# Performance work log

Measured on AMD Instinct MI355X. Metric: run time of the kernel, lower is better.

Reference implementation:

```python
import jax, jax.numpy as jnp
import numpy as np

N, E, HDIM, EDIM, MSG_H, UPD_H = 50000, 640000, 128, 32, 128, 128
LN_EPS = 1e-5


def setup_inputs() -> dict:
    key = jax.random.key(0)
    ks = jax.random.split(key, 12)
    def lin(k, fan_in, fan_out):
        return jax.random.normal(k, (fan_in, fan_out), dtype=jnp.float32) / np.sqrt(fan_in)
    h = jax.random.normal(ks[0], (N, HDIM), dtype=jnp.float32)
    edge_index = jax.random.randint(ks[1], (2, E), 0, N, dtype=jnp.int32)
    edge_attr = jax.random.normal(ks[2], (E, EDIM), dtype=jnp.float32)
    return {
        "h": h,
        "edge_index": edge_index,
        "edge_attr": edge_attr,
        # edge MLP: Linear(2*hdim+edim -> msg_hidden), ReLU, Linear(msg_hidden -> hdim)
        "ew1": lin(ks[3], 2 * HDIM + EDIM, MSG_H),
        "eb1": jnp.zeros((MSG_H,), jnp.float32),
        "ew2": lin(ks[4], MSG_H, HDIM),
        "eb2": jnp.zeros((HDIM,), jnp.float32),
        # node MLP: Linear(2*hdim -> upd_hidden), ReLU, Linear(upd_hidden -> hdim)
        "nw1": lin(ks[5], 2 * HDIM, UPD_H),
        "nb1": jnp.zeros((UPD_H,), jnp.float32),
        "nw2": lin(ks[6], UPD_H, HDIM),
        "nb2": jnp.zeros((HDIM,), jnp.float32),
        # LayerNorm(hdim)
        "gamma": jnp.ones((HDIM,), jnp.float32),
        "beta": jnp.zeros((HDIM,), jnp.float32),
    }


def reference(h, edge_index, edge_attr, ew1, eb1, ew2, eb2, nw1, nb1, nw2, nb2, gamma, beta):
    src, dst = edge_index[0], edge_index[1]
    # gather + concat -> edge MLP  (eval mode: dropout inactive, edge_dropout off)
    m_in = jnp.concatenate([h[src], h[dst], edge_attr], axis=1)       # [E, 2H+EDIM]
    m = jax.nn.relu(m_in @ ew1 + eb1) @ ew2 + eb2                     # [E, H]
    # scatter-add messages into destination nodes
    agg = jax.ops.segment_sum(m, dst, num_segments=h.shape[0])        # [N, H]
    # node update MLP
    u_in = jnp.concatenate([h, agg], axis=1)                          # [N, 2H]
    h_upd = jax.nn.relu(u_in @ nw1 + nb1) @ nw2 + nb2                 # [N, H]
    # residual + LayerNorm
    x = h + h_upd
    mu = jnp.mean(x, axis=-1, keepdims=True)
    var = jnp.mean(jnp.square(x - mu), axis=-1, keepdims=True)
    return (x - mu) * jax.lax.rsqrt(var + LN_EPS) * gamma + beta
```

## Files before the change

kernel.cpp:

```cpp
#include <hip/hip_runtime.h>
#include <cstdint>

#define HD 128
#define ED 32
#define BME 32
#define BMN 128
#define PAD_N 264
#define PAD_T 136
#define EGRID 512

typedef _Float16 f16;
typedef __attribute__((ext_vector_type(2))) _Float16 f16x2;
typedef __attribute__((ext_vector_type(4))) _Float16 f16x4;
typedef __attribute__((ext_vector_type(8))) _Float16 f16x8;
typedef __attribute__((ext_vector_type(4))) float    f32x4;
typedef __attribute__((ext_vector_type(4))) unsigned int u32x4;

__device__ __forceinline__ f32x4 mfma16(f16x8 a, f16x8 b, f32x4 c) {
    return __builtin_amdgcn_mfma_f32_16x16x32_f16(a, b, c, 0, 0, 0);
}
__device__ __forceinline__ f16x8 cvt8(const float* p) {
    const float4 a0 = *(const float4*)p;
    const float4 a1 = *(const float4*)(p + 4);
    f16x8 v;
    v[0] = (f16)a0.x; v[1] = (f16)a0.y; v[2] = (f16)a0.z; v[3] = (f16)a0.w;
    v[4] = (f16)a1.x; v[5] = (f16)a1.y; v[6] = (f16)a1.z; v[7] = (f16)a1.w;
    return v;
}
__device__ __forceinline__ void barrier_lds() {
    asm volatile("s_waitcnt lgkmcnt(0)" ::: "memory");
    __builtin_amdgcn_s_barrier();
    __builtin_amdgcn_sched_barrier(0);
}

__global__ __launch_bounds__(256) void zero_f32(float4* p, long n4) {
    long i = (long)blockIdx.x * blockDim.x + threadIdx.x;
    const long stride = (long)gridDim.x * blockDim.x;
    const float4 z = make_float4(0.f, 0.f, 0.f, 0.f);
    for (; i < n4; i += stride) p[i] = z;
}
__global__ __launch_bounds__(256) void zero_i32(int* p, int n) {
    int i = blockIdx.x * blockDim.x + threadIdx.x;
    if (i < n) p[i] = 0;
}
__global__ __launch_bounds__(256)
void cvt_f16_kernel(const float* __restrict__ x, f16* __restrict__ y, long n8) {
    long i = blockIdx.x * 256 + threadIdx.x;
    const long stride = (long)gridDim.x * 256;
    for (; i < n8; i += stride) *(f16x8*)(y + i * 8) = cvt8(x + i * 8);
}
__global__ __launch_bounds__(256)
void pack_all_kernel(const float* __restrict__ ew1, const float* __restrict__ ew2,
                     const float* __restrict__ nw1, const float* __restrict__ nw2,
                     f16* __restrict__ w1p, f16* __restrict__ w2p,
                     f16* __restrict__ n1p, f16* __restrict__ n2p)
{
    const int b = blockIdx.x;
    const float* w; f16* wp; int base;
    if (b < 18)      { w = ew1; wp = w1p; base = b; }
    else if (b < 26) { w = ew2; wp = w2p; base = b - 18; }
    else if (b < 42) { w = nw1; wp = n1p; base = b - 26; }
    else             { w = nw2; wp = n2p; base = b - 42; }
    const int idx = base * 256 + threadIdx.x;
    const int l  = idx & 63;
    const int fr = idx >> 6;
    const int wi = fr & 7, kt = fr >> 3;
    const int lii = l & 15, qq = l >> 4;
    const float* p = w + (size_t)(32 * kt + 8 * qq) * HD + 16 * wi + lii;
    f16x8 v;
#pragma unroll
    for (int e2 = 0; e2 < 8; ++e2) v[e2] = (f16)p[(size_t)e2 * HD];
    *(f16x8*)(wp + (size_t)idx * 8) = v;
}

__global__ __launch_bounds__(256)
void hist_kernel(const int* __restrict__ eidx, int* __restrict__ rank,
                 int* __restrict__ cnt, int E) {
    int e = blockIdx.x * 256 + threadIdx.x;
    if (e < E) rank[e] = atomicAdd(&cnt[eidx[E + e]], 1);
}
__global__ __launch_bounds__(256)
void scan1_kernel(const int* __restrict__ cnt, int* __restrict__ bsum, int N) {
    const int b = blockIdx.x, t = threadIdx.x;
    const int base = b * 1024 + t * 4;
    int s = 0;
#pragma unroll
    for (int j = 0; j < 4; ++j) { int i = base + j; s += (i < N) ? cnt[i] : 0; }
#pragma unroll
    for (int off = 1; off < 64; off <<= 1) s += __shfl_xor(s, off, 64);
    __shared__ int ws[4];
    if ((t & 63) == 0) ws[t >> 6] = s;
    __syncthreads();
    if (t == 0) bsum[b] = ws[0] + ws[1] + ws[2] + ws[3];
}
__global__ __launch_bounds__(256)
void scan2_kernel(const int* __restrict__ bsum, int* __restrict__ boff,
                  int* __restrict__ rs, int nb, int N) {
    const int t = threadIdx.x, lane = t & 63, w = t >> 6;
    int v = (t < nb) ? bsum[t] : 0;
    int incl = v;
#pragma unroll
    for (int off = 1; off < 64; off <<= 1) {
        int u = __shfl_up(incl, off, 64);
        if (lane >= off) incl += u;
    }
    __shared__ int ws[4];
    if (lane == 63) ws[w] = incl;
    __syncthreads();
    int wo = 0;
    for (int k = 0; k < w; ++k) wo += ws[k];
    const int excl = wo + incl - v;
    if (t < nb) boff[t] = excl;
    if (t == nb - 1) rs[N] = excl + v;
}
__global__ __launch_bounds__(256)
void scan3_kernel(const int* __restrict__ cnt, const int* __restrict__ boff,
                  int* __restrict__ rs, int N) {
    const int b = blockIdx.x, t = threadIdx.x;
    const int base = b * 1024 + t * 4;
    int v[4]; int ts = 0;
#pragma unroll
    for (int j = 0; j < 4; ++j) { int i = base + j; v[j] = (i < N) ? cnt[i] : 0; ts += v[j]; }
    const int lane = t & 63, w = t >> 6;
    int incl = ts;
#pragma unroll
    for (int off = 1; off < 64; off <<= 1) {
        int u = __shfl_up(incl, off, 64);
        if (lane >= off) incl += u;
    }
    __shared__ int ws[4];
    if (lane == 63) ws[w] = incl;
    __syncthreads();
    int wo = 0;
    for (int k = 0; k < w; ++k) wo += ws[k];
    int run = boff[b] + wo + incl - ts;
#pragma unroll
    for (int j = 0; j < 4; ++j) {
        int i = base + j;
        if (i < N) rs[i] = run;
        run += v[j];
    }
}
__global__ __launch_bounds__(256)
void pos_kernel(const int* __restrict__ eidx, const int* __restrict__ rs,
                const int* __restrict__ rank,
                int* __restrict__ esrc, int* __restrict__ edst,
                int* __restrict__ eea, int E) {
    int e = blockIdx.x * 256 + threadIdx.x;
    if (e < E) {
        const int dst = eidx[E + e];
        const int p = rs[dst] + rank[e];
        esrc[p] = eidx[e];
        edst[p] = dst;
        eea[p]  = e;
    }
}

template <int MODE>
__global__ __launch_bounds__(256, 2)
void edge_kernel(const f16*   __restrict__ h16,
                 const int*   __restrict__ eidx,
                 const float* __restrict__ ea,
                 const f16*   __restrict__ w1p,
                 const float* __restrict__ b1,
                 const f16*   __restrict__ w2p,
                 const float* __restrict__ b2,
                 void*        __restrict__ aggm,
                 const int*   __restrict__ esrc,
                 const int*   __restrict__ edst,
                 const int*   __restrict__ eea,
                 int E, int ntiles)
{
    __shared__ __align__(16) f16 sA [BME * 320];
    __shared__ __align__(16) f16 sT [BME * 128];
    __shared__ __align__(16) f16 sTo[BME * 128];
    __shared__ int sIdx[2][BME];

    const int t  = threadIdx.x;
    const int l  = t & 63;
    const int wv = t >> 6;
    const int li = l & 15;
    const int q  = l >> 4;
    const int lm = l & 7;
    const int r  = t >> 3;
    const int q8 = t & 7;

    f16x8 A1[2][9], A2[2][4];
#pragma unroll
    for (int ht = 0; ht < 2; ++ht) {
#pragma unroll
        for (int kt = 0; kt < 9; ++kt)
            A1[ht][kt] = *(const f16x8*)(w1p + ((size_t)(kt * 8 + wv * 2 + ht) * 64 + l) * 8);
#pragma unroll
        for (int kt = 0; kt < 4; ++kt)
            A2[ht][kt] = *(const f16x8*)(w2p + ((size_t)(kt * 8 + wv * 2 + ht) * 64 + l) * 8);
    }

    f16x8 d[4];
    f16x8 d4;
    int   psr = 0;
    auto prefetch = [&](int tile) {
        const int slot = min(tile * BME + r, E - 1);
        int src, dst, e;
        if (MODE == 0) {
            e = slot; src = eidx[e]; dst = eidx[E + e]; psr = dst;
        } else {
            src = esrc[slot]; dst = edst[slot]; e = eea[slot];
        }
        const f16* hs = h16 + (size_t)src * HD;
        const f16* hd = h16 + (size_t)dst * HD;
#pragma unroll
        for (int i = 0; i < 4; ++i) {
            const int c = (q8 + 8 * i) * 8;
            d[i] = (c < HD) ? *(const f16x8*)(hs + c)
                            : *(const f16x8*)(hd + (c - HD));
        }
        if (q8 < 4) d4 = cvt8(ea + (size_t)e * ED + q8 * 8);
    };

    int tb = blockIdx.x;
    if (tb < ntiles) prefetch(tb);
    int par = 0;

    for (; tb < ntiles; tb += gridDim.x, par ^= 1) {
        {
            f16* row = sA + r * 320;
            const int sw = r & 7;
#pragma unroll
            for (int i = 0; i < 4; ++i) {
                const int ch = q8 + 8 * i;
                *(f16x8*)(row + ((ch ^ sw) * 8)) = d[i];
            }
            if (q8 < 4)
                *(f16x8*)(row + (((q8 + 32) ^ sw) * 8)) = d4;
            if (MODE == 0 && q8 == 0) sIdx[par][r] = psr;
        }
        barrier_lds();

        const int nt = tb + (int)gridDim.x;
        if (nt < ntiles) prefetch(nt);

        f32x4 acc[2][2];
#pragma unroll
        for (int i = 0; i < 2; ++i)
#pragma unroll
            for (int j = 0; j < 2; ++j) acc[i][j] = (f32x4){0.f, 0.f, 0.f, 0.f};
#pragma unroll
        for (int kt = 0; kt < 9; ++kt) {
#pragma unroll
            for (int e = 0; e < 2; ++e) {
                const f16x8 b = *(const f16x8*)(sA + (16 * e + li) * 320
                                                + (((4 * kt + q) ^ lm) * 8));
                acc[0][e] = mfma16(A1[0][kt], b, acc[0][e]);
                acc[1][e] = mfma16(A1[1][kt], b, acc[1][e]);
            }
        }

#pragma unroll
        for (int ht = 0; ht < 2; ++ht) {
            const int hidb = 32 * wv + 16 * ht + 4 * q;
            const float4 bb = *(const float4*)(b1 + hidb);
            const int chT = hidb >> 3;
            const int off = hidb & 7;
#pragma unroll
            for (int e = 0; e < 2; ++e) {
                const f32x4 v = acc[ht][e];
                float x0 = fmaxf(v[0] + bb.x, 0.f), x1 = fmaxf(v[1] + bb.y, 0.f);
                float x2 = fmaxf(v[2] + bb.z, 0.f), x3 = fmaxf(v[3] + bb.w, 0.f);
                f16x4 o; o[0] = (f16)x0; o[1] = (f16)x1; o[2] = (f16)x2; o[3] = (f16)x3;
                *(f16x4*)(sT + (16 * e + li) * 128 + ((chT ^ lm) * 8) + off) = o;
            }
        }
        barrier_lds();

        f32x4 acc2[2][2];
#pragma unroll
        for (int i = 0; i < 2; ++i)
#pragma unroll
            for (int j = 0; j < 2; ++j) acc2[i][j] = (f32x4){0.f, 0.f, 0.f, 0.f};
#pragma unroll
        for (int kt = 0; kt < 4; ++kt) {
#pragma unroll
            for (int e = 0; e < 2; ++e) {
                const f16x8 b = *(const f16x8*)(sT + (16 * e + li) * 128
                                                + (((4 * kt + q) ^ lm) * 8));
                acc2[0][e] = mfma16(A2[0][kt], b, acc2[0][e]);
                acc2[1][e] = mfma16(A2[1][kt], b, acc2[1][e]);
            }
        }

        if (MODE == 0) {
            float* agg = (float*)aggm;
#pragma unroll
            for (int ht = 0; ht < 2; ++ht) {
                const int hidb = 32 * wv + 16 * ht + 4 * q;
                const float4 bb = *(const float4*)(b2 + hidb);
#pragma unroll
                for (int e = 0; e < 2; ++e) {
                    const int edge = 16 * e + li;
                    if (tb * BME + edge < E) {
                        float* p = agg + (size_t)sIdx[par][edge] * HD + hidb;
                        const f32x4 v = acc2[ht][e];
                        atomicAdd(p + 0, v[0] + bb.x);
                        atomicAdd(p + 1, v[1] + bb.y);
                        atomicAdd(p + 2, v[2] + bb.z);
                        atomicAdd(p + 3, v[3] + bb.w);
                    }
                }
            }
            barrier_lds();
        } else {
#pragma unroll
            for (int ht = 0; ht < 2; ++ht) {
                const int hidb = 32 * wv + 16 * ht + 4 * q;
                const float4 bb = *(const float4*)(b2 + hidb);
                const int chT = hidb >> 3;
                const int off = hidb & 7;
#pragma unroll
                for (int e = 0; e < 2; ++e) {
                    const f32x4 v = acc2[ht][e];
                    f16x4 o;
                    o[0] = (f16)(v[0] + bb.x); o[1] = (f16)(v[1] + bb.y);
                    o[2] = (f16)(v[2] + bb.z); o[3] = (f16)(v[3] + bb.w);
                    *(f16x4*)(sTo + (16 * e + li) * 128 + ((chT ^ lm) * 8) + off) = o;
                }
            }
            barrier_lds();
            f16* m = (f16*)aggm;
            const size_t mbase = (size_t)tb * BME * HD;
#pragma unroll
            for (int i = 0; i < 2; ++i) {
                const int idx  = t + i * 256;
                const int row2 = idx >> 4;
                const int c    = idx & 15;
                if (tb * BME + row2 < E) {
                    const f16x8 v = *(const f16x8*)(sTo + row2 * 128
                                                    + ((c ^ (row2 & 7)) * 8));
                    __builtin_nontemporal_store(*(const u32x4*)&v,
                        (u32x4*)(m + mbase + (size_t)row2 * HD + c * 8));
                }
            }
        }
    }
}

template <int CSR>
__global__ __launch_bounds__(256, 2)
void node_kernel(const f16*   __restrict__ h16,
                 const float* __restrict__ h,
                 const f16*   __restrict__ m,
                 const int*   __restrict__ rs,
                 const float* __restrict__ aggf,
                 const f16*   __restrict__ w1p,
                 const float* __restrict__ b1,
                 const f16*   __restrict__ w2p,
                 const float* __restrict__ b2,
                 const float* __restrict__ gamma,
                 const float* __restrict__ beta,
                 float*       __restrict__ out,
                 int N)
{
    __shared__ __align__(16) f16 sA[BMN * PAD_N];
    __shared__ float sMV[2 * BMN];

    const int t  = threadIdx.x;
    const int l  = t & 63;
    const int wv = t >> 6;
    const int li = l & 15;
    const int q  = l >> 4;
    const int nbase = blockIdx.x * BMN;

    {
        const int r = t >> 1, half = t & 1;
        const int node = min(nbase + r, N - 1);
        f16* rowp = sA + r * PAD_N;
        {
            const f16* srcp = h16 + (size_t)node * HD + half * 64;
#pragma unroll
            for (int i = 0; i < 8; ++i)
                *(f16x8*)(rowp + half * 64 + i * 8) = *(const f16x8*)(srcp + i * 8);
        }
        if (CSR) {
            const int s = rs[node], en = rs[node + 1];
            float ag[64];
#pragma unroll
            for (int i = 0; i < 64; ++i) ag[i] = 0.f;
            const f16* base = m + (size_t)s * HD + half * 64;
            for (int j = 0; j < en - s; ++j) {
                const f16* rp = base + (size_t)j * HD;
#pragma unroll
                for (int i = 0; i < 8; ++i) {
                    const f16x8 v = *(const f16x8*)(rp + i * 8);
#pragma unroll
                    for (int k2 = 0; k2 < 8; ++k2) ag[i * 8 + k2] += (float)v[k2];
                }
            }
#pragma unroll
            for (int i = 0; i < 8; ++i) {
                f16x8 o;
#pragma unroll
                for (int k2 = 0; k2 < 8; ++k2) o[k2] = (f16)ag[i * 8 + k2];
                *(f16x8*)(rowp + 128 + half * 64 + i * 8) = o;
            }
        } else {
            const float* srcp = aggf + (size_t)node * HD + half * 64;
#pragma unroll
            for (int i = 0; i < 8; ++i)
                *(f16x8*)(rowp + 128 + half * 64 + i * 8) = cvt8(srcp + i * 8);
        }
    }
    __syncthreads();

    f16x8 A1[2][8];
#pragma unroll
    for (int ht = 0; ht < 2; ++ht)
#pragma unroll
        for (int kt = 0; kt < 8; ++kt)
            A1[ht][kt] = *(const f16x8*)(w1p + ((size_t)(kt * 8 + wv * 2 + ht) * 64 + l) * 8);

    f32x4 acc[2][8];
#pragma unroll
    for (int i = 0; i < 2; ++i)
#pragma unroll
        for (int j = 0; j < 8; ++j) acc[i][j] = (f32x4){0.f, 0.f, 0.f, 0.f};
#pragma unroll
    for (int kt = 0; kt < 8; ++kt) {
#pragma unroll
        for (int et = 0; et < 8; ++et) {
            const f16x8 b = *(const f16x8*)(sA + (16 * et + li) * PAD_N + 32 * kt + 8 * q);
            acc[0][et] = mfma16(A1[0][kt], b, acc[0][et]);
            acc[1][et] = mfma16(A1[1][kt], b, acc[1][et]);
        }
    }
    __syncthreads();

    f16x8 A2[2][4];
#pragma unroll
    for (int ht = 0; ht < 2; ++ht)
#pragma unroll
        for (int kt = 0; kt < 4; ++kt)
            A2[ht][kt] = *(const f16x8*)(w2p + ((size_t)(kt * 8 + wv * 2 + ht) * 64 + l) * 8);

    f16* sT = sA;
#pragma unroll
    for (int ht = 0; ht < 2; ++ht) {
        const int hidb = 32 * wv + 16 * ht + 4 * q;
        const float4 bb = *(const float4*)(b1 + hidb);
#pragma unroll
        for (int et = 0; et < 8; ++et) {
            const f32x4 v = acc[ht][et];
            float x0 = fmaxf(v[0] + bb.x, 0.f), x1 = fmaxf(v[1] + bb.y, 0.f);
            float x2 = fmaxf(v[2] + bb.z, 0.f), x3 = fmaxf(v[3] + bb.w, 0.f);
            f16x4 o; o[0] = (f16)x0; o[1] = (f16)x1; o[2] = (f16)x2; o[3] = (f16)x3;
            *(f16x4*)(sT + (16 * et + li) * PAD_T + hidb) = o;
        }
    }
    __syncthreads();

    f32x4 acc2[2][8];
#pragma unroll
    for (int i = 0; i < 2; ++i)
#pragma unroll
        for (int j = 0; j < 8; ++j) acc2[i][j] = (f32x4){0.f, 0.f, 0.f, 0.f};
#pragma unroll
    for (int kt = 0; kt < 4; ++kt) {
#pragma unroll
        for (int et = 0; et < 8; ++et) {
            const f16x8 b = *(const f16x8*)(sT + (16 * et + li) * PAD_T + 32 * kt + 8 * q);
            acc2[0][et] = mfma16(A2[0][kt], b, acc2[0][et]);
            acc2[1][et] = mfma16(A2[1][kt], b, acc2[1][et]);
        }
    }
    __syncthreads();

    float* sX = (float*)sA;
#pragma unroll
    for (int ht = 0; ht < 2; ++ht) {
        const int hidb = 32 * wv + 16 * ht + 4 * q;
        const float4 bb = *(const float4*)(b2 + hidb);
#pragma unroll
        for (int et = 0; et < 8; ++et) {
            const int node = 16 * et + li;
            const int nc   = min(nbase + node, N - 1);
            const float4 hv = *(const float4*)(h + (size_t)nc * HD + hidb);
            const f32x4 v = acc2[ht][et];
            f32x4 x;
            x[0] = v[0] + bb.x + hv.x;
            x[1] = v[1] + bb.y + hv.y;
            x[2] = v[2] + bb.z + hv.z;
            x[3] = v[3] + bb.w + hv.w;
            *(f32x4*)(sX + (size_t)node * 132 + hidb) = x;
        }
    }
    __syncthreads();

    {
        const int node  = t >> 1;
        const int half2 = t & 1;
        const float* px = sX + node * 132 + half2 * 64;
        float s = 0.f, sq = 0.f;
#pragma unroll
        for (int i = 0; i < 16; ++i) {
            const float4 v = *(const float4*)(px + i * 4);
            s  += v.x + v.y + v.z + v.w;
            sq += v.x * v.x + v.y * v.y + v.z * v.z + v.w * v.w;
        }
        s  += __shfl_xor(s, 1);
        sq += __shfl_xor(sq, 1);
        if (!half2) {
            const float mean = s * (1.f / HD);
            const float var  = sq * (1.f / HD) - mean * mean;
            sMV[node]       = mean;
            sMV[BMN + node] = rsqrtf(var + 1e-5f);
        }
    }
    __syncthreads();

#pragma unroll
    for (int i = 0; i < 16; ++i) {
        const int idx  = t + i * 256;
        const int node = idx >> 5;
        const int c4   = (idx & 31) * 4;
        if (nbase + node < N) {
            const float4 xv = *(const float4*)(sX + node * 132 + c4);
            const float4 g4 = *(const float4*)(gamma + c4);
            const float4 b4 = *(const float4*)(beta + c4);
            const float mean = sMV[node];
            const float rstd = sMV[BMN + node];
            float4 o;
            o.x = (xv.x - mean) * rstd * g4.x + b4.x;
            o.y = (xv.y - mean) * rstd * g4.y + b4.y;
            o.z = (xv.z - mean) * rstd * g4.z + b4.z;
            o.w = (xv.w - mean) * rstd * g4.w + b4.w;
            *(float4*)(out + (size_t)(nbase + node) * HD + c4) = o;
        }
    }
}

extern "C" void kernel_launch(void* const* d_in, const int* in_sizes, int n_in,
                              void* d_out, int out_size, void* d_ws, size_t ws_size,
                              hipStream_t stream)
{
    const float* h     = (const float*)d_in[0];
    const int*   eidx  = (const int*)  d_in[1];
    const float* ea    = (const float*)d_in[2];
    const float* ew1   = (const float*)d_in[3];
    const float* eb1   = (const float*)d_in[4];
    const float* ew2   = (const float*)d_in[5];
    const float* eb2   = (const float*)d_in[6];
    const float* nw1   = (const float*)d_in[7];
    const float* nb1   = (const float*)d_in[8];
    const float* nw2   = (const float*)d_in[9];
    const float* nb2   = (const float*)d_in[10];
    const float* gamma = (const float*)d_in[11];
    const float* beta  = (const float*)d_in[12];
    float* out = (float*)d_out;

    const int N = in_sizes[0] / HD;
    const int E = in_sizes[1] / 2;
    const int ntiles = (E + BME - 1) / BME;
    const int nb = (N + 1023) / 1024;

    size_t off = 0;
    auto alloc = [&](size_t bytes) {
        size_t o = off; off += (bytes + 255) & ~(size_t)255; return o;
    };
    const size_t o_m    = alloc((size_t)E * HD * sizeof(f16));
    const size_t o_h16  = alloc((size_t)N * HD * sizeof(f16));
    const size_t o_rank = alloc((size_t)E * sizeof(int));
    const size_t o_es   = alloc((size_t)E * sizeof(int));
    const size_t o_ed   = alloc((size_t)E * sizeof(int));
    const size_t o_ee   = alloc((size_t)E * sizeof(int));
    const size_t o_rs   = alloc((size_t)(N + 1) * sizeof(int));
    const size_t o_cnt  = alloc((size_t)N * sizeof(int));
    const size_t o_bs   = alloc((size_t)(nb + 1) * sizeof(int));
    const size_t o_bo   = alloc((size_t)(nb + 1) * sizeof(int));
    const size_t o_w1p  = alloc((size_t)9 * 8 * 64 * 8 * sizeof(f16));
    const size_t o_w2p  = alloc((size_t)4 * 8 * 64 * 8 * sizeof(f16));
    const size_t o_n1p  = alloc((size_t)8 * 8 * 64 * 8 * sizeof(f16));
    const size_t o_n2p  = alloc((size_t)4 * 8 * 64 * 8 * sizeof(f16));
    const bool csr = (off <= ws_size) && (nb <= 256);
    char* ws = (char*)d_ws;

    if (csr) {
        f16* mb   = (f16*)(ws + o_m);
        f16* h16  = (f16*)(ws + o_h16);
        int* rank = (int*)(ws + o_rank);
        int* esrc = (int*)(ws + o_es);
        int* edst = (int*)(ws + o_ed);
        int* eea  = (int*)(ws + o_ee);
        int* rs   = (int*)(ws + o_rs);
        int* cnt  = (int*)(ws + o_cnt);
        int* bsum = (int*)(ws + o_bs);
        int* boff = (int*)(ws + o_bo);
        f16* w1p  = (f16*)(ws + o_w1p);
        f16* w2p  = (f16*)(ws + o_w2p);
        f16* n1p  = (f16*)(ws + o_n1p);
        f16* n2p  = (f16*)(ws + o_n2p);

        zero_i32<<<(N + 255) / 256, 256, 0, stream>>>(cnt, N);
        hist_kernel<<<(E + 255) / 256, 256, 0, stream>>>(eidx, rank, cnt, E);
        scan1_kernel<<<nb, 256, 0, stream>>>(cnt, bsum, N);
        scan2_kernel<<<1, 256, 0, stream>>>(bsum, boff, rs, nb, N);
        scan3_kernel<<<nb, 256, 0, stream>>>(cnt, boff, rs, N);
        pos_kernel<<<(E + 255) / 256, 256, 0, stream>>>(eidx, rs, rank, esrc, edst, eea, E);
        cvt_f16_kernel<<<2048, 256, 0, stream>>>(h, h16, (long)N * HD / 8);
        pack_all_kernel<<<50, 256, 0, stream>>>(ew1, ew2, nw1, nw2, w1p, w2p, n1p, n2p);
        edge_kernel<1><<<EGRID, 256, 0, stream>>>(
            h16, eidx, ea, w1p, eb1, w2p, eb2, (void*)mb, esrc, edst, eea, E, ntiles);
        node_kernel<1><<<(N + BMN - 1) / BMN, 256, 0, stream>>>(
            h16, h, mb, rs, nullptr, n1p, nb1, n2p, nb2, gamma, beta, out, N);
    } else {
        size_t foff = 0;
        auto falloc = [&](size_t bytes) {
            size_t o = foff; foff += (bytes + 255) & ~(size_t)255; return o;
        };
        float* agg = (float*)(ws + falloc((size_t)N * HD * sizeof(float)));
        f16*   h16 = (f16*)  (ws + falloc((size_t)N * HD * sizeof(f16)));
        f16*   w1p = (f16*)  (ws + falloc((size_t)9 * 8 * 64 * 8 * sizeof(f16)));
        f16*   w2p = (f16*)  (ws + falloc((size_t)4 * 8 * 64 * 8 * sizeof(f16)));
        f16*   n1p = (f16*)  (ws + falloc((size_t)8 * 8 * 64 * 8 * sizeof(f16)));
        f16*   n2p = (f16*)  (ws + falloc((size_t)4 * 8 * 64 * 8 * sizeof(f16)));

        zero_f32<<<1024, 256, 0, stream>>>((float4*)agg, (long)N * HD / 4);
        cvt_f16_kernel<<<2048, 256, 0, stream>>>(h, h16, (long)N * HD / 8);
        pack_all_kernel<<<50, 256, 0, stream>>>(ew1, ew2, nw1, nw2, w1p, w2p, n1p, n2p);
        edge_kernel<0><<<EGRID, 256, 0, stream>>>(
            h16, eidx, ea, w1p, eb1, w2p, eb2, (void*)agg,
            nullptr, nullptr, nullptr, E, ntiles);
        node_kernel<0><<<(N + BMN - 1) / BMN, 256, 0, stream>>>(
            h16, h, nullptr, nullptr, agg, n1p, nb1, n2p, nb2, gamma, beta, out, N);
    }
}
```

Measured before the change: 268.6 us.

## Reduce sorted edge messages in-tile and fix up tile boundaries instead of storing messages

In CSR mode the edge kernel now sums its dst-sorted messages in fp32 per destination within each 32-edge tile. It writes interior segment sums straight into agg and puts the first and last segment of each tile into a boundary buffer, which a new fixup kernel then combines across tiles. This removes the E×128 f16 message buffer write and its reread in the node kernel, at the cost of zeroing agg, an extra launch and a serial per-column scan in 128 threads. The edge grid also grows from 512 to 768 blocks.

```diff
diff --git a/kernel.cpp b/kernel.cpp
--- a/kernel.cpp
+++ b/kernel.cpp
@@ -7,14 +7,13 @@
 #define BMN 128
 #define PAD_N 264
 #define PAD_T 136
-#define EGRID 512
+#define EGRID 768
 
 typedef _Float16 f16;
 typedef __attribute__((ext_vector_type(2))) _Float16 f16x2;
 typedef __attribute__((ext_vector_type(4))) _Float16 f16x4;
 typedef __attribute__((ext_vector_type(8))) _Float16 f16x8;
 typedef __attribute__((ext_vector_type(4))) float    f32x4;
-typedef __attribute__((ext_vector_type(4))) unsigned int u32x4;
 
 __device__ __forceinline__ f32x4 mfma16(f16x8 a, f16x8 b, f32x4 c) {
     return __builtin_amdgcn_mfma_f32_16x16x32_f16(a, b, c, 0, 0, 0);
@@ -165,15 +164,17 @@
                  const float* __restrict__ b1,
                  const f16*   __restrict__ w2p,
                  const float* __restrict__ b2,
-                 void*        __restrict__ aggm,
+                 float*       __restrict__ agg,
+                 float*       __restrict__ bnd,
+                 int*         __restrict__ bndid,
                  const int*   __restrict__ esrc,
                  const int*   __restrict__ edst,
                  const int*   __restrict__ eea,
                  int E, int ntiles)
 {
-    __shared__ __align__(16) f16 sA [BME * 320];
-    __shared__ __align__(16) f16 sT [BME * 128];
-    __shared__ __align__(16) f16 sTo[BME * 128];
+    __shared__ __align__(16) f16   sA  [BME * 320];
+    __shared__ __align__(16) f16   sT  [BME * 128];
+    __shared__ __align__(16) float sToF[BME * 128];
     __shared__ int sIdx[2][BME];
 
     const int t  = threadIdx.x;
@@ -203,10 +204,11 @@
         const int slot = min(tile * BME + r, E - 1);
         int src, dst, e;
         if (MODE == 0) {
-            e = slot; src = eidx[e]; dst = eidx[E + e]; psr = dst;
+            e = slot; src = eidx[e]; dst = eidx[E + e];
         } else {
             src = esrc[slot]; dst = edst[slot]; e = eea[slot];
         }
+        psr = dst;
         const f16* hs = h16 + (size_t)src * HD;
         const f16* hd = h16 + (size_t)dst * HD;
 #pragma unroll
@@ -233,7 +235,7 @@
             }
             if (q8 < 4)
                 *(f16x8*)(row + (((q8 + 32) ^ sw) * 8)) = d4;
-            if (MODE == 0 && q8 == 0) sIdx[par][r] = psr;
+            if (q8 == 0) sIdx[par][r] = psr;
         }
         barrier_lds();
 
@@ -290,7 +292,6 @@
         }
 
         if (MODE == 0) {
-            float* agg = (float*)aggm;
 #pragma unroll
             for (int ht = 0; ht < 2; ++ht) {
                 const int hidb = 32 * wv + 16 * ht + 4 * q;
@@ -314,42 +315,79 @@
             for (int ht = 0; ht < 2; ++ht) {
                 const int hidb = 32 * wv + 16 * ht + 4 * q;
                 const float4 bb = *(const float4*)(b2 + hidb);
-                const int chT = hidb >> 3;
-                const int off = hidb & 7;
+                const int ch = hidb >> 2;
 #pragma unroll
                 for (int e = 0; e < 2; ++e) {
+                    const int row = 16 * e + li;
                     const f32x4 v = acc2[ht][e];
-                    f16x4 o;
-                    o[0] = (f16)(v[0] + bb.x); o[1] = (f16)(v[1] + bb.y);
-                    o[2] = (f16)(v[2] + bb.z); o[3] = (f16)(v[3] + bb.w);
-                    *(f16x4*)(sTo + (16 * e + li) * 128 + ((chT ^ lm) * 8) + off) = o;
+                    f32x4 x;
+                    x[0] = v[0] + bb.x; x[1] = v[1] + bb.y;
+                    x[2] = v[2] + bb.z; x[3] = v[3] + bb.w;
+                    *(f32x4*)(sToF + row * 128 + ((ch ^ ((row & 7) << 2)) << 2)) = x;
                 }
             }
             barrier_lds();
-            f16* m = (f16*)aggm;
-            const size_t mbase = (size_t)tb * BME * HD;
-#pragma unroll
-            for (int i = 0; i < 2; ++i) {
-                const int idx  = t + i * 256;
-                const int row2 = idx >> 4;
-                const int c    = idx & 15;
-                if (tb * BME + row2 < E) {
-                    const f16x8 v = *(const f16x8*)(sTo + row2 * 128
-                                                    + ((c ^ (row2 & 7)) * 8));
-                    __builtin_nontemporal_store(*(const u32x4*)&v,
-                        (u32x4*)(m + mbase + (size_t)row2 * HD + c * 8));
+
+            if (t < 128) {
+                const int col  = t;
+                const int ch   = col >> 2;
+                const int co   = col & 3;
+                const int sLast = min(BME - 1, E - 1 - tb * BME);
+                float run = 0.f;
+                int   rdst = sIdx[par][0];
+                bool  touches0 = true;
+                for (int s = 0; s <= sLast; ++s) {
+                    const int ds = sIdx[par][s];
+                    if (ds != rdst) {
+                        if (touches0) {
+                            bnd[((size_t)2 * tb) * HD + col] = run;
+                            if (col == 0) bndid[2 * tb] = rdst;
+                        } else {
+                            agg[(size_t)rdst * HD + col] = run;
+                        }
+                        run = 0.f; rdst = ds; touches0 = false;
+                    }
+                    run += sToF[s * 128 + ((ch ^ ((s & 7) << 2)) << 2) + co];
+                }
+                if (touches0) {
+                    bnd[((size_t)2 * tb) * HD + col]     = run;
+                    bnd[((size_t)2 * tb + 1) * HD + col] = 0.f;
+                    if (col == 0) { bndid[2 * tb] = rdst; bndid[2 * tb + 1] = rdst; }
+                } else {
+                    bnd[((size_t)2 * tb + 1) * HD + col] = run;
+                    if (col == 0) bndid[2 * tb + 1] = rdst;
                 }
             }
         }
     }
 }
 
-template <int CSR>
+__global__ __launch_bounds__(256)
+void fixup_kernel(const float* __restrict__ bnd, const int* __restrict__ bndid,
+                  float* __restrict__ agg, int nent)
+{
+    const int lane = threadIdx.x & 63;
+    int i = blockIdx.x * 4 + (threadIdx.x >> 6);
+    const int stride = gridDim.x * 4;
+    for (; i < nent; i += stride) {
+        const int d = bndid[i];
+        if (i > 0 && bndid[i - 1] == d) continue;
+        float s0 = bnd[(size_t)i * HD + lane];
+        float s1 = bnd[(size_t)i * HD + 64 + lane];
+        int j = i + 1;
+        while (j < nent && bndid[j] == d) {
+            s0 += bnd[(size_t)j * HD + lane];
+            s1 += bnd[(size_t)j * HD + 64 + lane];
+            ++j;
+        }
+        agg[(size_t)d * HD + lane]      = s0;
+        agg[(size_t)d * HD + 64 + lane] = s1;
+    }
+}
+
 __global__ __launch_bounds__(256, 2)
 void node_kernel(const f16*   __restrict__ h16,
                  const float* __restrict__ h,
-                 const f16*   __restrict__ m,
-                 const int*   __restrict__ rs,
                  const float* __restrict__ aggf,
                  const f16*   __restrict__ w1p,
                  const float* __restrict__ b1,
@@ -380,29 +418,7 @@
             for (int i = 0; i < 8; ++i)
                 *(f16x8*)(rowp + half * 64 + i * 8) = *(const f16x8*)(srcp + i * 8);
         }
-        if (CSR) {
-            const int s = rs[node], en = rs[node + 1];
-            float ag[64];
-#pragma unroll
-            for (int i = 0; i < 64; ++i) ag[i] = 0.f;
-            const f16* base = m + (size_t)s * HD + half * 64;
-            for (int j = 0; j < en - s; ++j) {
-                const f16* rp = base + (size_t)j * HD;
-#pragma unroll
-                for (int i = 0; i < 8; ++i) {
-                    const f16x8 v = *(const f16x8*)(rp + i * 8);
-#pragma unroll
-                    for (int k2 = 0; k2 < 8; ++k2) ag[i * 8 + k2] += (float)v[k2];
-                }
-            }
-#pragma unroll
-            for (int i = 0; i < 8; ++i) {
-                f16x8 o;
-#pragma unroll
-                for (int k2 = 0; k2 < 8; ++k2) o[k2] = (f16)ag[i * 8 + k2];
-                *(f16x8*)(rowp + 128 + half * 64 + i * 8) = o;
-            }
-        } else {
+        {
             const float* srcp = aggf + (size_t)node * HD + half * 64;
 #pragma unroll
             for (int i = 0; i < 8; ++i)
@@ -565,8 +581,10 @@
     auto alloc = [&](size_t bytes) {
         size_t o = off; off += (bytes + 255) & ~(size_t)255; return o;
     };
-    const size_t o_m    = alloc((size_t)E * HD * sizeof(f16));
+    const size_t o_agg  = alloc((size_t)N * HD * sizeof(float));
     const size_t o_h16  = alloc((size_t)N * HD * sizeof(f16));
+    const size_t o_bnd  = alloc((size_t)2 * ntiles * HD * sizeof(float));
+    const size_t o_bid  = alloc((size_t)2 * ntiles * sizeof(int));
     const size_t o_rank = alloc((size_t)E * sizeof(int));
     const size_t o_es   = alloc((size_t)E * sizeof(int));
     const size_t o_ed   = alloc((size_t)E * sizeof(int));
@@ -582,22 +600,26 @@
     const bool csr = (off <= ws_size) && (nb <= 256);
     char* ws = (char*)d_ws;
 
+    float* agg = (float*)(ws + o_agg);
+    f16*   h16 = (f16*)(ws + o_h16);
+    f16*   w1p = (f16*)(ws + o_w1p);
+    f16*   w2p = (f16*)(ws + o_w2p);
+    f16*   n1p = (f16*)(ws + o_n1p);
+    f16*   n2p = (f16*)(ws + o_n2p);
+
     if (csr) {
-        f16* mb   = (f16*)(ws + o_m);
-        f16* h16  = (f16*)(ws + o_h16);
-        int* rank = (int*)(ws + o_rank);
-        int* esrc = (int*)(ws + o_es);
-        int* edst = (int*)(ws + o_ed);
-        int* eea  = (int*)(ws + o_ee);
-        int* rs   = (int*)(ws + o_rs);
-        int* cnt  = (int*)(ws + o_cnt);
-        int* bsum = (int*)(ws + o_bs);
-        int* boff = (int*)(ws + o_bo);
-        f16* w1p  = (f16*)(ws + o_w1p);
-        f16* w2p  = (f16*)(ws + o_w2p);
-        f16* n1p  = (f16*)(ws + o_n1p);
-        f16* n2p  = (f16*)(ws + o_n2p);
-
+        float* bnd  = (float*)(ws + o_bnd);
+        int* bndid  = (int*)(ws + o_bid);
+        int* rank   = (int*)(ws + o_rank);
+        int* esrc   = (int*)(ws + o_es);
+        int* edst   = (int*)(ws + o_ed);
+        int* eea    = (int*)(ws + o_ee);
+        int* rs     = (int*)(ws + o_rs);
+        int* cnt    = (int*)(ws + o_cnt);
+        int* bsum   = (int*)(ws + o_bs);
+        int* boff   = (int*)(ws + o_bo);
+
+        zero_f32<<<1024, 256, 0, stream>>>((float4*)agg, (long)N * HD / 4);
         zero_i32<<<(N + 255) / 256, 256, 0, stream>>>(cnt, N);
         hist_kernel<<<(E + 255) / 256, 256, 0, stream>>>(eidx, rank, cnt, E);
         scan1_kernel<<<nb, 256, 0, stream>>>(cnt, bsum, N);
@@ -607,28 +629,19 @@
         cvt_f16_kernel<<<2048, 256, 0, stream>>>(h, h16, (long)N * HD / 8);
         pack_all_kernel<<<50, 256, 0, stream>>>(ew1, ew2, nw1, nw2, w1p, w2p, n1p, n2p);
         edge_kernel<1><<<EGRID, 256, 0, stream>>>(
-            h16, eidx, ea, w1p, eb1, w2p, eb2, (void*)mb, esrc, edst, eea, E, ntiles);
-        node_kernel<1><<<(N + BMN - 1) / BMN, 256, 0, stream>>>(
-            h16, h, mb, rs, nullptr, n1p, nb1, n2p, nb2, gamma, beta, out, N);
+            h16, eidx, ea, w1p, eb1, w2p, eb2, agg, bnd, bndid,
+            esrc, edst, eea, E, ntiles);
+        fixup_kernel<<<(2 * ntiles + 3) / 4, 256, 0, stream>>>(bnd, bndid, agg, 2 * ntiles);
+        node_kernel<<<(N + BMN - 1) / BMN, 256, 0, stream>>>(
+            h16, h, agg, n1p, nb1, n2p, nb2, gamma, beta, out, N);
     } else {
-        size_t foff = 0;
-        auto falloc = [&](size_t bytes) {
-            size_t o = foff; foff += (bytes + 255) & ~(size_t)255; return o;
-        };
-        float* agg = (float*)(ws + falloc((size_t)N * HD * sizeof(float)));
-        f16*   h16 = (f16*)  (ws + falloc((size_t)N * HD * sizeof(f16)));
-        f16*   w1p = (f16*)  (ws + falloc((size_t)9 * 8 * 64 * 8 * sizeof(f16)));
-        f16*   w2p = (f16*)  (ws + falloc((size_t)4 * 8 * 64 * 8 * sizeof(f16)));
-        f16*   n1p = (f16*)  (ws + falloc((size_t)8 * 8 * 64 * 8 * sizeof(f16)));
-        f16*   n2p = (f16*)  (ws + falloc((size_t)4 * 8 * 64 * 8 * sizeof(f16)));
-
         zero_f32<<<1024, 256, 0, stream>>>((float4*)agg, (long)N * HD / 4);
         cvt_f16_kernel<<<2048, 256, 0, stream>>>(h, h16, (long)N * HD / 8);
         pack_all_kernel<<<50, 256, 0, stream>>>(ew1, ew2, nw1, nw2, w1p, w2p, n1p, n2p);
         edge_kernel<0><<<EGRID, 256, 0, stream>>>(
-            h16, eidx, ea, w1p, eb1, w2p, eb2, (void*)agg,
+            h16, eidx, ea, w1p, eb1, w2p, eb2, agg, nullptr, nullptr,
             nullptr, nullptr, nullptr, E, ntiles);
-        node_kernel<0><<<(N + BMN - 1) / BMN, 256, 0, stream>>>(
-            h16, h, nullptr, nullptr, agg, n1p, nb1, n2p, nb2, gamma, beta, out, N);
-    }
-}
+        node_kernel<<<(N + BMN - 1) / BMN, 256, 0, stream>>>(
+            h16, h, agg, n1p, nb1, n2p, nb2, gamma, beta, out, N);
+    }
+}
```

Result: slower. 402.9 us (+50.0%).
